# Performance work log

Measured on AMD Instinct MI355X. Metric: run time of the kernel, lower is better.

## Reference

```python
import jax, jax.numpy as jnp
import numpy as np

N_NODES = 50000
N_EDGES = 800000
D_IN = 256
D_HID = 128
NUM_LAYERS = 6
ALPHA = 0.1
THETA = 0.5
EPS = 1e-5  # BatchNorm1d default eps


def setup_inputs() -> dict:
    key = jax.random.key(0)
    ks = jax.random.split(key, 6)
    x = jax.random.normal(ks[0], (N_NODES, D_IN), dtype=jnp.float32)
    edge_index = jax.random.randint(ks[1], (2, N_EDGES), 0, N_NODES)
    # GCNConv(D_IN, D_HID): weight + bias
    W_lin = jax.random.normal(ks[2], (D_IN, D_HID), dtype=jnp.float32) / np.sqrt(D_IN).astype(np.float32)
    b_lin = jnp.zeros((D_HID,), jnp.float32)
    # GCN2Conv weight1 per layer (shared_weights=True -> only weight1, no bias)
    W1s = jax.random.normal(ks[3], (NUM_LAYERS - 1, D_HID, D_HID), dtype=jnp.float32) / np.sqrt(D_HID).astype(np.float32)
    # BatchNorm1d affine params per intermediate layer
    bn_gamma = jnp.ones((NUM_LAYERS - 2, D_HID), jnp.float32)
    bn_beta = jnp.zeros((NUM_LAYERS - 2, D_HID), jnp.float32)
    return {"x": x, "edge_index": edge_index, "W_lin": W_lin, "b_lin": b_lin,
            "W1s": W1s, "bn_gamma": bn_gamma, "bn_beta": bn_beta}


def _gcn_conv(x, W, b, edge_index):
    # PyG GCNConv: transform, add self-loops, D^{-1/2}(A+I)D^{-1/2} aggregation.
    n = x.shape[0]
    xw = x @ W  # [N, D_HID]
    loop = jnp.arange(n)
    src = jnp.concatenate([edge_index[0], loop])
    dst = jnp.concatenate([edge_index[1], loop])
    deg = jax.ops.segment_sum(jnp.ones(src.shape, xw.dtype), dst, num_segments=n)
    dinv = jax.lax.rsqrt(jnp.maximum(deg, 1.0))  # deg >= 1 thanks to self loops
    w = dinv[src] * dinv[dst]  # [E+N]
    return jax.ops.segment_sum(xw[src] * w[:, None], dst, num_segments=n) + b


def _gcn2_conv(z, x0, W1, edge_index, beta):
    # GCN2Conv with normalize=False, shared_weights=True:
    # h = (1-alpha)*sum_{j->i} z_j + alpha*x0 ; out = (1-beta)*h + beta*(h @ W1)
    n = z.shape[0]
    agg = jax.ops.segment_sum(z[edge_index[0]], edge_index[1], num_segments=n)
    h = (1.0 - ALPHA) * agg + ALPHA * x0
    return (1.0 - beta) * h + beta * (h @ W1)


def _batchnorm(z, gamma, beta_p):
    # training-mode BatchNorm1d over the node dimension (biased variance)
    mu = jnp.mean(z, axis=0)
    var = jnp.var(z, axis=0)
    return (z - mu) * jax.lax.rsqrt(var + EPS) * gamma + beta_p


def reference(x, edge_index, W_lin, b_lin, W1s, bn_gamma, bn_beta):
    z = _gcn_conv(x, W_lin, b_lin, edge_index)
    x0 = z
    n_convs = NUM_LAYERS - 1
    # GCN2Conv layer index l = i+1 -> beta_l = log(theta/l + 1)
    betas = [float(np.log(THETA / (i + 1) + 1.0)) for i in range(n_convs)]
    for i in range(n_convs):  # dropout=0.0 -> identity, omitted
        z = _gcn2_conv(z, x0, W1s[i], edge_index, betas[i])
        if i < n_convs - 1:
            z = _batchnorm(z, bn_gamma[i], bn_beta[i])
            z = jax.nn.relu(z)
    return z
```

## Files before the change

kernel.cpp:

```cpp
#include <hip/hip_runtime.h>
#include <math.h>

#define N_NODES 50000
#define N_EDGES 800000
#define D_IN 256
#define D_HID 128
#define ALPHA 0.1f
#define EPS 1e-5f

#define NBUCK 391
#define EPB 4096
#define NBLK 196

typedef __attribute__((ext_vector_type(8))) short bf16x8;
typedef __attribute__((ext_vector_type(4))) float f32x4;

static __device__ __forceinline__ unsigned short f2bf(float f) {
    unsigned int x = __float_as_uint(f);
    return (unsigned short)((x + 0x7fffu + ((x >> 16) & 1u)) >> 16);
}
static __device__ __forceinline__ float blo(unsigned int v) {
    return __uint_as_float(v << 16);
}
static __device__ __forceinline__ float bhi(unsigned int v) {
    return __uint_as_float(v & 0xffff0000u);
}
static __device__ __forceinline__ void unpack8(uint4 u, float* f) {
    f[0] = blo(u.x); f[1] = bhi(u.x);
    f[2] = blo(u.y); f[3] = bhi(u.y);
    f[4] = blo(u.z); f[5] = bhi(u.z);
    f[6] = blo(u.w); f[7] = bhi(u.w);
}

__global__ __launch_bounds__(256) void k_hist(const int* __restrict__ dst,
                                              int* __restrict__ hist, int e) {
    __shared__ int h[NBUCK];
    int t = threadIdx.x;
    for (int i = t; i < NBUCK; i += 256) h[i] = 0;
    __syncthreads();
    int base = blockIdx.x * EPB;
    int lim = e - base;
    if (lim > EPB) lim = EPB;
    for (int i = t; i < lim; i += 256) atomicAdd(&h[dst[base + i] >> 7], 1);
    __syncthreads();
    for (int i = t; i < NBUCK; i += 256) hist[blockIdx.x * NBUCK + i] = h[i];
}

__global__ __launch_bounds__(256) void k_bkscan(const int* __restrict__ hist,
                                                int* __restrict__ offsT, int* __restrict__ btot) {
    __shared__ int sh[256];
    int b = blockIdx.x;
    int t = threadIdx.x;
    int v = (t < NBLK) ? hist[t * NBUCK + b] : 0;
    sh[t] = v;
    __syncthreads();
    for (int ofs = 1; ofs < 256; ofs <<= 1) {
        int y = (t >= ofs) ? sh[t - ofs] : 0;
        __syncthreads();
        sh[t] += y;
        __syncthreads();
    }
    if (t < NBLK) offsT[b * NBLK + t] = sh[t] - v;
    if (t == 255) btot[b] = sh[255];
}

__global__ __launch_bounds__(512) void k_bbase(const int* __restrict__ btot,
                                               int* __restrict__ bbase, int* __restrict__ rp) {
    __shared__ int sh[512];
    int t = threadIdx.x;
    int v = (t < NBUCK) ? btot[t] : 0;
    sh[t] = v;
    __syncthreads();
    for (int ofs = 1; ofs < 512; ofs <<= 1) {
        int y = (t >= ofs) ? sh[t - ofs] : 0;
        __syncthreads();
        sh[t] += y;
        __syncthreads();
    }
    if (t < NBUCK) bbase[t] = sh[t] - v;
    if (t == 0) rp[N_NODES] = N_EDGES;
}

__global__ __launch_bounds__(256) void k_scatter(const int* __restrict__ src,
                                                 const int* __restrict__ dst,
                                                 const int* __restrict__ offsT,
                                                 const int* __restrict__ bbase,
                                                 unsigned int* __restrict__ buck, int e) {
    __shared__ int h[NBUCK];
    int t = threadIdx.x;
    for (int i = t; i < NBUCK; i += 256) h[i] = 0;
    __syncthreads();
    int base = blockIdx.x * EPB;
    int lim = e - base;
    if (lim > EPB) lim = EPB;
    for (int i = t; i < lim; i += 256) {
        int d = dst[base + i];
        int s = src[base + i];
        int b = d >> 7;
        int lp = atomicAdd(&h[b], 1);
        int pos = bbase[b] + offsT[b * NBLK + blockIdx.x] + lp;
        buck[pos] = (unsigned int)s | ((unsigned int)(d & 127) << 16);
    }
}

__global__ __launch_bounds__(256) void k_csr(const unsigned int* __restrict__ buck,
                                             const int* __restrict__ bbase,
                                             const int* __restrict__ btot,
                                             int* __restrict__ rp, float* __restrict__ dinv,
                                             int* __restrict__ cs) {
    __shared__ int dcnt[128];
    __shared__ int doff[128];
    int b = blockIdx.x;
    int t = threadIdx.x;
    if (t < 128) dcnt[t] = 0;
    __syncthreads();
    int base = bbase[b];
    int tot = btot[b];
    for (int i = t; i < tot; i += 256) {
        unsigned int v = buck[base + i];
        atomicAdd(&dcnt[(v >> 16) & 127], 1);
    }
    __syncthreads();
    if (t < 128) doff[t] = dcnt[t];
    __syncthreads();
    for (int ofs = 1; ofs < 128; ofs <<= 1) {
        int y = 0;
        if (t < 128 && t >= ofs) y = doff[t - ofs];
        __syncthreads();
        if (t < 128) doff[t] += y;
        __syncthreads();
    }
    int gd0 = b << 7;
    if (t < 128) {
        int ex = doff[t] - dcnt[t];
        if (gd0 + t < N_NODES) {
            rp[gd0 + t] = base + ex;
            dinv[gd0 + t] = rsqrtf((float)(dcnt[t] + 1));
        }
        dcnt[t] = ex;
    }
    __syncthreads();
    for (int i = t; i < tot; i += 256) {
        unsigned int v = buck[base + i];
        int p = atomicAdd(&dcnt[(v >> 16) & 127], 1);
        cs[base + p] = (int)(v & 0xffffu);
    }
}

__global__ __launch_bounds__(256) void k_prep_w(const float* __restrict__ W_lin,
                                                const float* __restrict__ W1s,
                                                unsigned short* __restrict__ Wlt,
                                                unsigned short* __restrict__ Wt) {
    int idx = blockIdx.x * 256 + threadIdx.x;
    if (idx < 128 * 256) {
        int c = idx >> 8, k = idx & 255;
        Wlt[idx] = f2bf(W_lin[k * 128 + c]);
    } else {
        int j = idx - 128 * 256;
        if (j < 5 * 128 * 128) {
            int l = j >> 14;
            int rem = j & 16383;
            int c = rem >> 7, k = rem & 127;
            float bet = logf(0.5f / (float)(l + 1) + 1.0f);
            float v = bet * W1s[l * 16384 + k * 128 + c];
            if (c == k) v += 1.0f - bet;
            Wt[j] = f2bf(v);
        }
    }
}

template <int K>
__global__ __launch_bounds__(256) void k_mgemm(const float* __restrict__ A,
                                               const unsigned short* __restrict__ Bt,
                                               unsigned short* __restrict__ outb, int M) {
    __shared__ short lds[2 * 128 * 136];
    short* As = lds;
    short* Bs = lds + 128 * 136;

    int t = threadIdx.x;
    int lane = t & 63;
    int wave = t >> 6;
    int wr = wave >> 1, wc = wave & 1;
    int row0 = blockIdx.x * 128;

    f32x4 acc[4][4];
#pragma unroll
    for (int m = 0; m < 4; ++m)
#pragma unroll
        for (int n = 0; n < 4; ++n) acc[m][n] = (f32x4){0.f, 0.f, 0.f, 0.f};

    int sr = t >> 1;
    int sh = t & 1;

    for (int k0 = 0; k0 < K; k0 += 128) {
        {
            int gr = row0 + sr;
            float4 zf = {0.f, 0.f, 0.f, 0.f};
            const float4* gp = (const float4*)(A + (size_t)gr * K + k0 + sh * 64);
#pragma unroll
            for (int u = 0; u < 8; ++u) {
                float4 a = (gr < M) ? gp[2 * u] : zf;
                float4 b = (gr < M) ? gp[2 * u + 1] : zf;
                uint4 w;
                w.x = (unsigned int)f2bf(a.x) | ((unsigned int)f2bf(a.y) << 16);
                w.y = (unsigned int)f2bf(a.z) | ((unsigned int)f2bf(a.w) << 16);
                w.z = (unsigned int)f2bf(b.x) | ((unsigned int)f2bf(b.y) << 16);
                w.w = (unsigned int)f2bf(b.z) | ((unsigned int)f2bf(b.w) << 16);
                *(uint4*)(As + sr * 136 + sh * 64 + u * 8) = w;
            }
        }
        {
            const uint4* gp = (const uint4*)(Bt + (size_t)sr * K + k0 + sh * 64);
#pragma unroll
            for (int u = 0; u < 8; ++u) {
                *(uint4*)(Bs + sr * 136 + sh * 64 + u * 8) = gp[u];
            }
        }
        __syncthreads();

#pragma unroll
        for (int ks = 0; ks < 4; ++ks) {
            bf16x8 af[4], bfr[4];
#pragma unroll
            for (int m = 0; m < 4; ++m)
                af[m] = *(const bf16x8*)(As + (wr * 64 + m * 16 + (lane & 15)) * 136 + ks * 32 + (lane >> 4) * 8);
#pragma unroll
            for (int n = 0; n < 4; ++n)
                bfr[n] = *(const bf16x8*)(Bs + (wc * 64 + n * 16 + (lane & 15)) * 136 + ks * 32 + (lane >> 4) * 8);
#pragma unroll
            for (int m = 0; m < 4; ++m)
#pragma unroll
                for (int n = 0; n < 4; ++n)
                    acc[m][n] = __builtin_amdgcn_mfma_f32_16x16x32_bf16(af[m], bfr[n], acc[m][n], 0, 0, 0);
        }
        __syncthreads();
    }

    short* Z = lds;
#pragma unroll
    for (int m = 0; m < 4; ++m)
#pragma unroll
        for (int n = 0; n < 4; ++n)
#pragma unroll
            for (int r = 0; r < 4; ++r) {
                int rl = wr * 64 + m * 16 + (lane >> 4) * 4 + r;
                int cl = wc * 64 + n * 16 + (lane & 15);
                Z[rl * 136 + cl] = (short)f2bf(acc[m][n][r]);
            }
    __syncthreads();
    int gr = row0 + sr;
    if (gr < M) {
#pragma unroll
        for (int u = 0; u < 8; ++u)
            *(uint4*)(outb + (size_t)gr * 128 + sh * 64 + u * 8) = *(uint4*)(Z + sr * 136 + sh * 64 + u * 8);
    }
}

template <int MODE>
__global__ __launch_bounds__(256) void k_lgemm(const unsigned short* __restrict__ A,
                                               const unsigned short* __restrict__ Bt,
                                               unsigned short* __restrict__ outb,
                                               float* __restrict__ outf,
                                               float* __restrict__ bn_s, float* __restrict__ bn_q,
                                               int M) {
    __shared__ short As[128 * 136];
    int t = threadIdx.x;
    int lane = t & 63;
    int wave = t >> 6;
    int wr = wave >> 1, wc = wave & 1;
    int row0 = blockIdx.x * 128;

    bf16x8 bfr[4][4];
#pragma unroll
    for (int ks = 0; ks < 4; ++ks)
#pragma unroll
        for (int n = 0; n < 4; ++n)
            bfr[ks][n] = *(const bf16x8*)(Bt + (size_t)(wc * 64 + n * 16 + (lane & 15)) * 128 + ks * 32 + (lane >> 4) * 8);

    int sr = t >> 1, sh = t & 1;
    {
        int gr = row0 + sr;
        uint4 zero = {0, 0, 0, 0};
        const uint4* gp = (const uint4*)(A + (size_t)gr * 128 + sh * 64);
#pragma unroll
        for (int u = 0; u < 8; ++u) {
            uint4 v = (gr < M) ? gp[u] : zero;
            *(uint4*)(As + sr * 136 + sh * 64 + u * 8) = v;
        }
    }
    __syncthreads();

    f32x4 acc[4][4];
#pragma unroll
    for (int m = 0; m < 4; ++m)
#pragma unroll
        for (int n = 0; n < 4; ++n) acc[m][n] = (f32x4){0.f, 0.f, 0.f, 0.f};

#pragma unroll
    for (int ks = 0; ks < 4; ++ks) {
        bf16x8 af[4];
#pragma unroll
        for (int m = 0; m < 4; ++m)
            af[m] = *(const bf16x8*)(As + (wr * 64 + m * 16 + (lane & 15)) * 136 + ks * 32 + (lane >> 4) * 8);
#pragma unroll
        for (int m = 0; m < 4; ++m)
#pragma unroll
            for (int n = 0; n < 4; ++n)
                acc[m][n] = __builtin_amdgcn_mfma_f32_16x16x32_bf16(af[m], bfr[ks][n], acc[m][n], 0, 0, 0);
    }

    if (MODE == 1) {
        float sum[4] = {0.f, 0.f, 0.f, 0.f}, sq[4] = {0.f, 0.f, 0.f, 0.f};
#pragma unroll
        for (int n = 0; n < 4; ++n)
#pragma unroll
            for (int m = 0; m < 4; ++m)
#pragma unroll
                for (int r = 0; r < 4; ++r) {
                    float v = acc[m][n][r];
                    sum[n] += v;
                    sq[n] += v * v;
                }
#pragma unroll
        for (int n = 0; n < 4; ++n) {
            sum[n] += __shfl_xor(sum[n], 16);
            sum[n] += __shfl_xor(sum[n], 32);
            sq[n] += __shfl_xor(sq[n], 16);
            sq[n] += __shfl_xor(sq[n], 32);
        }
        if (lane < 16) {
#pragma unroll
            for (int n = 0; n < 4; ++n) {
                int col = wc * 64 + n * 16 + lane;
                atomicAdd(&bn_s[col], sum[n]);
                atomicAdd(&bn_q[col], sq[n]);
            }
        }
    }

    if (MODE == 2) {
#pragma unroll
        for (int m = 0; m < 4; ++m)
#pragma unroll
            for (int n = 0; n < 4; ++n)
#pragma unroll
                for (int r = 0; r < 4; ++r) {
                    int gr = row0 + wr * 64 + m * 16 + (lane >> 4) * 4 + r;
                    int cl = wc * 64 + n * 16 + (lane & 15);
                    if (gr < M) outf[(size_t)gr * 128 + cl] = acc[m][n][r];
                }
    } else {
        __syncthreads();
        short* Z = As;
#pragma unroll
        for (int m = 0; m < 4; ++m)
#pragma unroll
            for (int n = 0; n < 4; ++n)
#pragma unroll
                for (int r = 0; r < 4; ++r) {
                    int rl = wr * 64 + m * 16 + (lane >> 4) * 4 + r;
                    int cl = wc * 64 + n * 16 + (lane & 15);
                    Z[rl * 136 + cl] = (short)f2bf(acc[m][n][r]);
                }
        __syncthreads();
        int gr = row0 + sr;
        if (gr < M) {
#pragma unroll
            for (int u = 0; u < 8; ++u)
                *(uint4*)(outb + (size_t)gr * 128 + sh * 64 + u * 8) = *(uint4*)(Z + sr * 136 + sh * 64 + u * 8);
        }
    }
}

template <int MODE>
__global__ __launch_bounds__(256) void k_agg(const uint4* __restrict__ src4,
                                             const uint4* __restrict__ x04,
                                             const int* __restrict__ rp, const int* __restrict__ cs,
                                             const float* __restrict__ dinv,
                                             const float* __restrict__ b_lin,
                                             const float* __restrict__ st,
                                             uint4* __restrict__ dst4,
                                             float* __restrict__ bns, int n) {
    if (blockIdx.x == 0) bns[threadIdx.x] = 0.f;

    int wid = (blockIdx.x * 256 + threadIdx.x) >> 6;
    int lane = threadIdx.x & 63;
    if (wid >= n) return;
    int q = lane >> 4;
    int c = lane & 15;

    int start = __builtin_amdgcn_readfirstlane(rp[wid]);
    int end = __builtin_amdgcn_readfirstlane(rp[wid + 1]);

    float sc[8], tc[8];
    if (MODE == 2) {
        float4 s0 = ((const float4*)st)[c * 2];
        float4 s1 = ((const float4*)st)[c * 2 + 1];
        float4 t0 = ((const float4*)st)[32 + c * 2];
        float4 t1 = ((const float4*)st)[32 + c * 2 + 1];
        sc[0] = s0.x; sc[1] = s0.y; sc[2] = s0.z; sc[3] = s0.w;
        sc[4] = s1.x; sc[5] = s1.y; sc[6] = s1.z; sc[7] = s1.w;
        tc[0] = t0.x; tc[1] = t0.y; tc[2] = t0.z; tc[3] = t0.w;
        tc[4] = t1.x; tc[5] = t1.y; tc[6] = t1.z; tc[7] = t1.w;
    }
    float dn = (MODE == 0) ? dinv[wid] : 0.f;

    float acc[8];
#pragma unroll
    for (int i = 0; i < 8; ++i) acc[i] = 0.f;

#define ACCUM(vv, ww)                                                     \
    {                                                                     \
        float f_[8];                                                      \
        unpack8(vv, f_);                                                  \
        if (MODE == 0) {                                                  \
            _Pragma("unroll") for (int i_ = 0; i_ < 8; ++i_)              \
                acc[i_] = fmaf(ww, f_[i_], acc[i_]);                      \
        } else if (MODE == 1) {                                           \
            _Pragma("unroll") for (int i_ = 0; i_ < 8; ++i_)              \
                acc[i_] += f_[i_];                                        \
        } else {                                                          \
            _Pragma("unroll") for (int i_ = 0; i_ < 8; ++i_)              \
                acc[i_] += fmaxf(fmaf(sc[i_], f_[i_], tc[i_]), 0.f);      \
        }                                                                 \
    }

    for (int base = start; base < end; base += 64) {
        int cnt = end - base;
        if (cnt > 64) cnt = 64;
        int myi = cs[base + ((lane < cnt) ? lane : 0)];
        float myw = (MODE == 0) ? dinv[myi] : 0.f;

        int j = 0;
        for (; j + 15 < cnt; j += 16) {
            int s0 = __shfl(myi, j + q);
            int s1 = __shfl(myi, j + 4 + q);
            int s2 = __shfl(myi, j + 8 + q);
            int s3 = __shfl(myi, j + 12 + q);
            uint4 v0 = src4[(size_t)s0 * 16 + c];
            uint4 v1 = src4[(size_t)s1 * 16 + c];
            uint4 v2 = src4[(size_t)s2 * 16 + c];
            uint4 v3 = src4[(size_t)s3 * 16 + c];
            float w0 = 0.f, w1 = 0.f, w2 = 0.f, w3 = 0.f;
            if (MODE == 0) {
                w0 = __shfl(myw, j + q) * dn;
                w1 = __shfl(myw, j + 4 + q) * dn;
                w2 = __shfl(myw, j + 8 + q) * dn;
                w3 = __shfl(myw, j + 12 + q) * dn;
            }
            ACCUM(v0, w0);
            ACCUM(v1, w1);
            ACCUM(v2, w2);
            ACCUM(v3, w3);
        }
        for (; j + 7 < cnt; j += 8) {
            int s0 = __shfl(myi, j + q);
            int s1 = __shfl(myi, j + 4 + q);
            uint4 v0 = src4[(size_t)s0 * 16 + c];
            uint4 v1 = src4[(size_t)s1 * 16 + c];
            float w0 = 0.f, w1 = 0.f;
            if (MODE == 0) {
                w0 = __shfl(myw, j + q) * dn;
                w1 = __shfl(myw, j + 4 + q) * dn;
            }
            ACCUM(v0, w0);
            ACCUM(v1, w1);
        }
        for (; j + 3 < cnt; j += 4) {
            int s0 = __shfl(myi, j + q);
            uint4 v0 = src4[(size_t)s0 * 16 + c];
            float w0 = 0.f;
            if (MODE == 0) w0 = __shfl(myw, j + q) * dn;
            ACCUM(v0, w0);
        }
        int rem = cnt - j;
        if (rem > 0) {
            int jj = j + q;
            bool act = jj < cnt;
            int jsafe = act ? jj : (cnt - 1);
            int s0 = __shfl(myi, jsafe);
            uint4 v0 = src4[(size_t)s0 * 16 + c];
            float m = act ? 1.f : 0.f;
            if (MODE == 0) {
                float w0 = __shfl(myw, jsafe) * dn * m;
                ACCUM(v0, w0);
            } else {
                float f_[8];
                unpack8(v0, f_);
                if (MODE == 1) {
#pragma unroll
                    for (int i_ = 0; i_ < 8; ++i_) acc[i_] = fmaf(m, f_[i_], acc[i_]);
                } else {
#pragma unroll
                    for (int i_ = 0; i_ < 8; ++i_)
                        acc[i_] = fmaf(m, fmaxf(fmaf(sc[i_], f_[i_], tc[i_]), 0.f), acc[i_]);
                }
            }
        }
    }
#undef ACCUM

#pragma unroll
    for (int i = 0; i < 8; ++i) {
        acc[i] += __shfl_xor(acc[i], 16);
        acc[i] += __shfl_xor(acc[i], 32);
    }

    if (MODE == 0) {
        uint4 sv = src4[(size_t)wid * 16 + c];
        float fs[8];
        unpack8(sv, fs);
        float w2 = dn * dn;
        float4 b0 = ((const float4*)b_lin)[c * 2];
        float4 b1 = ((const float4*)b_lin)[c * 2 + 1];
        float bb[8] = {b0.x, b0.y, b0.z, b0.w, b1.x, b1.y, b1.z, b1.w};
#pragma unroll
        for (int i = 0; i < 8; ++i) acc[i] = fmaf(w2, fs[i], acc[i]) + bb[i];
    } else {
        uint4 xv = x04[(size_t)wid * 16 + c];
        float fx[8];
        unpack8(xv, fx);
#pragma unroll
        for (int i = 0; i < 8; ++i) acc[i] = fmaf(ALPHA, fx[i], (1.0f - ALPHA) * acc[i]);
    }

    if (lane < 16) {
        uint4 o;
        o.x = (unsigned int)f2bf(acc[0]) | ((unsigned int)f2bf(acc[1]) << 16);
        o.y = (unsigned int)f2bf(acc[2]) | ((unsigned int)f2bf(acc[3]) << 16);
        o.z = (unsigned int)f2bf(acc[4]) | ((unsigned int)f2bf(acc[5]) << 16);
        o.w = (unsigned int)f2bf(acc[6]) | ((unsigned int)f2bf(acc[7]) << 16);
        dst4[(size_t)wid * 16 + c] = o;
    }
}

__global__ void k_bn_fin(const float* __restrict__ bn_s, const float* __restrict__ bn_q,
                         const float* __restrict__ gamma, const float* __restrict__ betap,
                         float* __restrict__ st, int n) {
    int c = threadIdx.x;
    float inv_n = 1.0f / (float)n;
    float mu = bn_s[c] * inv_n;
    float var = bn_q[c] * inv_n - mu * mu;
    var = fmaxf(var, 0.f);
    float s = gamma[c] * rsqrtf(var + EPS);
    st[c] = s;
    st[128 + c] = betap[c] - mu * s;
}

extern "C" void kernel_launch(void* const* d_in, const int* in_sizes, int n_in,
                              void* d_out, int out_size, void* d_ws, size_t ws_size,
                              hipStream_t stream) {
    const float* x = (const float*)d_in[0];
    const int* ei = (const int*)d_in[1];
    const float* W_lin = (const float*)d_in[2];
    const float* b_lin = (const float*)d_in[3];
    const float* W1s = (const float*)d_in[4];
    const float* gam = (const float*)d_in[5];
    const float* betp = (const float*)d_in[6];
    float* out = (float*)d_out;

    char* ws = (char*)d_ws;
    size_t off = 0;
    auto alloc = [&](size_t b) { size_t p = off; off = (off + b + 255) & ~(size_t)255; return p; };
    int* rp = (int*)(ws + alloc((size_t)(N_NODES + 1) * 4));
    int* cs = (int*)(ws + alloc((size_t)N_EDGES * 4));
    float* dinv = (float*)(ws + alloc((size_t)N_NODES * 4));
    int* hist = (int*)(ws + alloc((size_t)NBLK * NBUCK * 4));
    int* offsT = (int*)(ws + alloc((size_t)NBUCK * NBLK * 4));
    int* btot = (int*)(ws + alloc((size_t)NBUCK * 4));
    int* bbase = (int*)(ws + alloc((size_t)NBUCK * 4));
    unsigned int* buck = (unsigned int*)(ws + alloc((size_t)N_EDGES * 4));
    unsigned short* xwb = (unsigned short*)(ws + alloc((size_t)N_NODES * D_HID * 2));
    unsigned short* x0b = (unsigned short*)(ws + alloc((size_t)N_NODES * D_HID * 2));
    unsigned short* zb = (unsigned short*)(ws + alloc((size_t)N_NODES * D_HID * 2));
    unsigned short* hb = (unsigned short*)(ws + alloc((size_t)N_NODES * D_HID * 2));
    unsigned short* Wlt = (unsigned short*)(ws + alloc((size_t)128 * 256 * 2));
    unsigned short* Wt = (unsigned short*)(ws + alloc((size_t)5 * 128 * 128 * 2));
    float* bns = (float*)(ws + alloc(256 * 4));
    float* st = (float*)(ws + alloc(256 * 4));

    const int ggrid = (N_NODES + 127) / 128;
    const int agrid = (N_NODES + 3) / 4;

    k_hist<<<NBLK, 256, 0, stream>>>(ei + N_EDGES, hist, N_EDGES);
    k_bkscan<<<NBUCK, 256, 0, stream>>>(hist, offsT, btot);
    k_bbase<<<1, 512, 0, stream>>>(btot, bbase, rp);
    k_scatter<<<NBLK, 256, 0, stream>>>(ei, ei + N_EDGES, offsT, bbase, buck, N_EDGES);
    k_csr<<<NBUCK, 256, 0, stream>>>(buck, bbase, btot, rp, dinv, cs);

    k_prep_w<<<(128 * 256 + 5 * 128 * 128 + 255) / 256, 256, 0, stream>>>(W_lin, W1s, Wlt, Wt);

    k_mgemm<D_IN><<<ggrid, 256, 0, stream>>>(x, Wlt, xwb, N_NODES);
    k_agg<0><<<agrid, 256, 0, stream>>>((const uint4*)xwb, nullptr, rp, cs, dinv, b_lin,
                                        nullptr, (uint4*)x0b, bns, N_NODES);

    for (int i = 0; i < 5; ++i) {
        const unsigned short* zsrc = (i == 0) ? x0b : zb;
        if (i == 0)
            k_agg<1><<<agrid, 256, 0, stream>>>((const uint4*)zsrc, (const uint4*)x0b,
                                                rp, cs, nullptr, nullptr, nullptr,
                                                (uint4*)hb, bns, N_NODES);
        else
            k_agg<2><<<agrid, 256, 0, stream>>>((const uint4*)zsrc, (const uint4*)x0b,
                                                rp, cs, nullptr, nullptr, st,
                                                (uint4*)hb, bns, N_NODES);
        const unsigned short* W1 = Wt + (size_t)i * 128 * 128;
        if (i < 4) {
            k_lgemm<1><<<ggrid, 256, 0, stream>>>(hb, W1, zb, nullptr, bns, bns + 128, N_NODES);
            k_bn_fin<<<1, 128, 0, stream>>>(bns, bns + 128, gam + (size_t)i * 128,
                                            betp + (size_t)i * 128, st, N_NODES);
        } else {
            k_lgemm<2><<<ggrid, 256, 0, stream>>>(hb, W1, nullptr, out, nullptr, nullptr, N_NODES);
        }
    }
}
```

Measured before the change: 432.5 us.

## Unify GEMMs into 64-row tiled kernel and pre-cast input to bf16

Replaces the two GEMM kernels with one templated kernel that uses 64-row tiles, with each wave owning 16 rows across all 128 columns. This doubles the grid size for better occupancy and CU coverage. The fp32 input x is now converted to bf16 by a separate cast kernel, which moves the conversion out of the GEMM load path. That costs an extra read and write of the full x matrix. BatchNorm statistics are reduced in LDS before the atomics, and the fp32 output store goes through LDS for coalescing.

Result: no change. 435.2 us (+0.6%).

```diff
diff --git a/kernel.cpp b/kernel.cpp
--- a/kernel.cpp
+++ b/kernel.cpp
@@ -144,6 +144,20 @@
         unsigned int v = buck[base + i];
         int p = atomicAdd(&dcnt[(v >> 16) & 127], 1);
         cs[base + p] = (int)(v & 0xffffu);
+    }
+}
+
+__global__ __launch_bounds__(256) void k_cast_x(const float4* __restrict__ x, ushort2* __restrict__ xb,
+                                                int n4) {
+    int i = blockIdx.x * 256 + threadIdx.x;
+    if (i < n4) {
+        float4 v = x[i];
+        ushort2 a;
+        a.x = f2bf(v.x); a.y = f2bf(v.y);
+        ushort2 b;
+        b.x = f2bf(v.z); b.y = f2bf(v.w);
+        xb[i * 2] = a;
+        xb[i * 2 + 1] = b;
     }
 }
 
@@ -169,205 +183,116 @@
     }
 }
 
-template <int K>
-__global__ __launch_bounds__(256) void k_mgemm(const float* __restrict__ A,
-                                               const unsigned short* __restrict__ Bt,
-                                               unsigned short* __restrict__ outb, int M) {
-    __shared__ short lds[2 * 128 * 136];
+template <int K, int MODE>
+__global__ __launch_bounds__(256) void k_gemm(const unsigned short* __restrict__ A,
+                                              const unsigned short* __restrict__ Bt,
+                                              unsigned short* __restrict__ outb,
+                                              float* __restrict__ outf,
+                                              float* __restrict__ bn_s, float* __restrict__ bn_q,
+                                              int M) {
+    __shared__ short lds[64 * 136 + 128 * 136];
     short* As = lds;
-    short* Bs = lds + 128 * 136;
+    short* Bs = lds + 64 * 136;
 
     int t = threadIdx.x;
     int lane = t & 63;
-    int wave = t >> 6;
-    int wr = wave >> 1, wc = wave & 1;
-    int row0 = blockIdx.x * 128;
-
-    f32x4 acc[4][4];
-#pragma unroll
-    for (int m = 0; m < 4; ++m)
-#pragma unroll
-        for (int n = 0; n < 4; ++n) acc[m][n] = (f32x4){0.f, 0.f, 0.f, 0.f};
-
-    int sr = t >> 1;
-    int sh = t & 1;
+    int w = t >> 6;
+    int c16 = lane & 15;
+    int q16 = lane >> 4;
+    int row0 = blockIdx.x * 64;
+
+    f32x4 acc[8];
+#pragma unroll
+    for (int n = 0; n < 8; ++n) acc[n] = (f32x4){0.f, 0.f, 0.f, 0.f};
+
+    int ar = t >> 2, aq = t & 3;
+    int br = t >> 1, bh = t & 1;
 
     for (int k0 = 0; k0 < K; k0 += 128) {
         {
-            int gr = row0 + sr;
-            float4 zf = {0.f, 0.f, 0.f, 0.f};
-            const float4* gp = (const float4*)(A + (size_t)gr * K + k0 + sh * 64);
-#pragma unroll
-            for (int u = 0; u < 8; ++u) {
-                float4 a = (gr < M) ? gp[2 * u] : zf;
-                float4 b = (gr < M) ? gp[2 * u + 1] : zf;
-                uint4 w;
-                w.x = (unsigned int)f2bf(a.x) | ((unsigned int)f2bf(a.y) << 16);
-                w.y = (unsigned int)f2bf(a.z) | ((unsigned int)f2bf(a.w) << 16);
-                w.z = (unsigned int)f2bf(b.x) | ((unsigned int)f2bf(b.y) << 16);
-                w.w = (unsigned int)f2bf(b.z) | ((unsigned int)f2bf(b.w) << 16);
-                *(uint4*)(As + sr * 136 + sh * 64 + u * 8) = w;
+            int gr = row0 + ar;
+            uint4 z4 = {0, 0, 0, 0};
+            const uint4* gp = (const uint4*)(A + (size_t)gr * K + k0);
+#pragma unroll
+            for (int v = 0; v < 4; ++v) {
+                uint4 x4 = (gr < M) ? gp[aq * 4 + v] : z4;
+                *(uint4*)(As + ar * 136 + (aq * 4 + v) * 8) = x4;
             }
         }
         {
-            const uint4* gp = (const uint4*)(Bt + (size_t)sr * K + k0 + sh * 64);
-#pragma unroll
-            for (int u = 0; u < 8; ++u) {
-                *(uint4*)(Bs + sr * 136 + sh * 64 + u * 8) = gp[u];
+            const uint4* gp = (const uint4*)(Bt + (size_t)br * K + k0);
+#pragma unroll
+            for (int v = 0; v < 8; ++v)
+                *(uint4*)(Bs + br * 136 + (bh * 8 + v) * 8) = gp[bh * 8 + v];
+        }
+        __syncthreads();
+
+#pragma unroll
+        for (int ks = 0; ks < 4; ++ks) {
+            bf16x8 af = *(const bf16x8*)(As + (w * 16 + c16) * 136 + ks * 32 + q16 * 8);
+#pragma unroll
+            for (int n = 0; n < 8; ++n) {
+                bf16x8 bf = *(const bf16x8*)(Bs + (n * 16 + c16) * 136 + ks * 32 + q16 * 8);
+                acc[n] = __builtin_amdgcn_mfma_f32_16x16x32_bf16(af, bf, acc[n], 0, 0, 0);
             }
         }
         __syncthreads();
-
-#pragma unroll
-        for (int ks = 0; ks < 4; ++ks) {
-            bf16x8 af[4], bfr[4];
-#pragma unroll
-            for (int m = 0; m < 4; ++m)
-                af[m] = *(const bf16x8*)(As + (wr * 64 + m * 16 + (lane & 15)) * 136 + ks * 32 + (lane >> 4) * 8);
-#pragma unroll
-            for (int n = 0; n < 4; ++n)
-                bfr[n] = *(const bf16x8*)(Bs + (wc * 64 + n * 16 + (lane & 15)) * 136 + ks * 32 + (lane >> 4) * 8);
-#pragma unroll
-            for (int m = 0; m < 4; ++m)
-#pragma unroll
-                for (int n = 0; n < 4; ++n)
-                    acc[m][n] = __builtin_amdgcn_mfma_f32_16x16x32_bf16(af[m], bfr[n], acc[m][n], 0, 0, 0);
-        }
-        __syncthreads();
-    }
-
-    short* Z = lds;
-#pragma unroll
-    for (int m = 0; m < 4; ++m)
-#pragma unroll
-        for (int n = 0; n < 4; ++n)
-#pragma unroll
-            for (int r = 0; r < 4; ++r) {
-                int rl = wr * 64 + m * 16 + (lane >> 4) * 4 + r;
-                int cl = wc * 64 + n * 16 + (lane & 15);
-                Z[rl * 136 + cl] = (short)f2bf(acc[m][n][r]);
+    }
+
+    if (MODE == 2) {
+        float* Zf = (float*)lds;
+#pragma unroll
+        for (int n = 0; n < 8; ++n)
+#pragma unroll
+            for (int r = 0; r < 4; ++r)
+                Zf[(w * 16 + q16 * 4 + r) * 132 + n * 16 + c16] = acc[n][r];
+        __syncthreads();
+        int zr = t >> 2, zq = t & 3;
+        int gr = row0 + zr;
+        if (gr < M) {
+#pragma unroll
+            for (int v = 0; v < 8; ++v)
+                *(float4*)(outf + (size_t)gr * 128 + (zq * 8 + v) * 4) =
+                    *(float4*)(Zf + zr * 132 + (zq * 8 + v) * 4);
+        }
+    } else {
+        short* Z = As;
+        float* Sf = (float*)Bs;
+#pragma unroll
+        for (int n = 0; n < 8; ++n)
+#pragma unroll
+            for (int r = 0; r < 4; ++r)
+                Z[(w * 16 + q16 * 4 + r) * 136 + n * 16 + c16] = (short)f2bf(acc[n][r]);
+        if (MODE == 1) {
+#pragma unroll
+            for (int n = 0; n < 8; ++n) {
+                float s = acc[n][0] + acc[n][1] + acc[n][2] + acc[n][3];
+                float qq = acc[n][0] * acc[n][0] + acc[n][1] * acc[n][1] +
+                           acc[n][2] * acc[n][2] + acc[n][3] * acc[n][3];
+                s += __shfl_xor(s, 16);
+                s += __shfl_xor(s, 32);
+                qq += __shfl_xor(qq, 16);
+                qq += __shfl_xor(qq, 32);
+                if (lane < 16) {
+                    Sf[w * 128 + n * 16 + lane] = s;
+                    Sf[512 + w * 128 + n * 16 + lane] = qq;
+                }
             }
-    __syncthreads();
-    int gr = row0 + sr;
-    if (gr < M) {
-#pragma unroll
-        for (int u = 0; u < 8; ++u)
-            *(uint4*)(outb + (size_t)gr * 128 + sh * 64 + u * 8) = *(uint4*)(Z + sr * 136 + sh * 64 + u * 8);
-    }
-}
-
-template <int MODE>
-__global__ __launch_bounds__(256) void k_lgemm(const unsigned short* __restrict__ A,
-                                               const unsigned short* __restrict__ Bt,
-                                               unsigned short* __restrict__ outb,
-                                               float* __restrict__ outf,
-                                               float* __restrict__ bn_s, float* __restrict__ bn_q,
-                                               int M) {
-    __shared__ short As[128 * 136];
-    int t = threadIdx.x;
-    int lane = t & 63;
-    int wave = t >> 6;
-    int wr = wave >> 1, wc = wave & 1;
-    int row0 = blockIdx.x * 128;
-
-    bf16x8 bfr[4][4];
-#pragma unroll
-    for (int ks = 0; ks < 4; ++ks)
-#pragma unroll
-        for (int n = 0; n < 4; ++n)
-            bfr[ks][n] = *(const bf16x8*)(Bt + (size_t)(wc * 64 + n * 16 + (lane & 15)) * 128 + ks * 32 + (lane >> 4) * 8);
-
-    int sr = t >> 1, sh = t & 1;
-    {
-        int gr = row0 + sr;
-        uint4 zero = {0, 0, 0, 0};
-        const uint4* gp = (const uint4*)(A + (size_t)gr * 128 + sh * 64);
-#pragma unroll
-        for (int u = 0; u < 8; ++u) {
-            uint4 v = (gr < M) ? gp[u] : zero;
-            *(uint4*)(As + sr * 136 + sh * 64 + u * 8) = v;
-        }
-    }
-    __syncthreads();
-
-    f32x4 acc[4][4];
-#pragma unroll
-    for (int m = 0; m < 4; ++m)
-#pragma unroll
-        for (int n = 0; n < 4; ++n) acc[m][n] = (f32x4){0.f, 0.f, 0.f, 0.f};
-
-#pragma unroll
-    for (int ks = 0; ks < 4; ++ks) {
-        bf16x8 af[4];
-#pragma unroll
-        for (int m = 0; m < 4; ++m)
-            af[m] = *(const bf16x8*)(As + (wr * 64 + m * 16 + (lane & 15)) * 136 + ks * 32 + (lane >> 4) * 8);
-#pragma unroll
-        for (int m = 0; m < 4; ++m)
-#pragma unroll
-            for (int n = 0; n < 4; ++n)
-                acc[m][n] = __builtin_amdgcn_mfma_f32_16x16x32_bf16(af[m], bfr[ks][n], acc[m][n], 0, 0, 0);
-    }
-
-    if (MODE == 1) {
-        float sum[4] = {0.f, 0.f, 0.f, 0.f}, sq[4] = {0.f, 0.f, 0.f, 0.f};
-#pragma unroll
-        for (int n = 0; n < 4; ++n)
-#pragma unroll
-            for (int m = 0; m < 4; ++m)
-#pragma unroll
-                for (int r = 0; r < 4; ++r) {
-                    float v = acc[m][n][r];
-                    sum[n] += v;
-                    sq[n] += v * v;
-                }
-#pragma unroll
-        for (int n = 0; n < 4; ++n) {
-            sum[n] += __shfl_xor(sum[n], 16);
-            sum[n] += __shfl_xor(sum[n], 32);
-            sq[n] += __shfl_xor(sq[n], 16);
-            sq[n] += __shfl_xor(sq[n], 32);
-        }
-        if (lane < 16) {
-#pragma unroll
-            for (int n = 0; n < 4; ++n) {
-                int col = wc * 64 + n * 16 + lane;
-                atomicAdd(&bn_s[col], sum[n]);
-                atomicAdd(&bn_q[col], sq[n]);
-            }
-        }
-    }
-
-    if (MODE == 2) {
-#pragma unroll
-        for (int m = 0; m < 4; ++m)
-#pragma unroll
-            for (int n = 0; n < 4; ++n)
-#pragma unroll
-                for (int r = 0; r < 4; ++r) {
-                    int gr = row0 + wr * 64 + m * 16 + (lane >> 4) * 4 + r;
-                    int cl = wc * 64 + n * 16 + (lane & 15);
-                    if (gr < M) outf[(size_t)gr * 128 + cl] = acc[m][n][r];
-                }
-    } else {
-        __syncthreads();
-        short* Z = As;
-#pragma unroll
-        for (int m = 0; m < 4; ++m)
-#pragma unroll
-            for (int n = 0; n < 4; ++n)
-#pragma unroll
-                for (int r = 0; r < 4; ++r) {
-                    int rl = wr * 64 + m * 16 + (lane >> 4) * 4 + r;
-                    int cl = wc * 64 + n * 16 + (lane & 15);
-                    Z[rl * 136 + cl] = (short)f2bf(acc[m][n][r]);
-                }
-        __syncthreads();
-        int gr = row0 + sr;
+        }
+        __syncthreads();
+        int zr = t >> 2, zq = t & 3;
+        int gr = row0 + zr;
         if (gr < M) {
 #pragma unroll
-            for (int u = 0; u < 8; ++u)
-                *(uint4*)(outb + (size_t)gr * 128 + sh * 64 + u * 8) = *(uint4*)(Z + sr * 136 + sh * 64 + u * 8);
+            for (int v = 0; v < 4; ++v)
+                *(uint4*)(outb + (size_t)gr * 128 + (zq * 4 + v) * 8) =
+                    *(uint4*)(Z + zr * 136 + (zq * 4 + v) * 8);
+        }
+        if (MODE == 1 && t < 128) {
+            float s = Sf[t] + Sf[128 + t] + Sf[256 + t] + Sf[384 + t];
+            float qq = Sf[512 + t] + Sf[640 + t] + Sf[768 + t] + Sf[896 + t];
+            atomicAdd(&bn_s[t], s);
+            atomicAdd(&bn_q[t], qq);
         }
     }
 }
@@ -570,6 +495,7 @@
     int* btot = (int*)(ws + alloc((size_t)NBUCK * 4));
     int* bbase = (int*)(ws + alloc((size_t)NBUCK * 4));
     unsigned int* buck = (unsigned int*)(ws + alloc((size_t)N_EDGES * 4));
+    unsigned short* xb = (unsigned short*)(ws + alloc((size_t)N_NODES * D_IN * 2));
     unsigned short* xwb = (unsigned short*)(ws + alloc((size_t)N_NODES * D_HID * 2));
     unsigned short* x0b = (unsigned short*)(ws + alloc((size_t)N_NODES * D_HID * 2));
     unsigned short* zb = (unsigned short*)(ws + alloc((size_t)N_NODES * D_HID * 2));
@@ -579,7 +505,7 @@
     float* bns = (float*)(ws + alloc(256 * 4));
     float* st = (float*)(ws + alloc(256 * 4));
 
-    const int ggrid = (N_NODES + 127) / 128;
+    const int ggrid = (N_NODES + 63) / 64;
     const int agrid = (N_NODES + 3) / 4;
 
     k_hist<<<NBLK, 256, 0, stream>>>(ei + N_EDGES, hist, N_EDGES);
@@ -588,9 +514,11 @@
     k_scatter<<<NBLK, 256, 0, stream>>>(ei, ei + N_EDGES, offsT, bbase, buck, N_EDGES);
     k_csr<<<NBUCK, 256, 0, stream>>>(buck, bbase, btot, rp, dinv, cs);
 
+    k_cast_x<<<(N_NODES * D_IN / 4 + 255) / 256, 256, 0, stream>>>((const float4*)x, (ushort2*)xb,
+                                                                   N_NODES * D_IN / 4);
     k_prep_w<<<(128 * 256 + 5 * 128 * 128 + 255) / 256, 256, 0, stream>>>(W_lin, W1s, Wlt, Wt);
 
-    k_mgemm<D_IN><<<ggrid, 256, 0, stream>>>(x, Wlt, xwb, N_NODES);
+    k_gemm<D_IN, 0><<<ggrid, 256, 0, stream>>>(xb, Wlt, xwb, nullptr, nullptr, nullptr, N_NODES);
     k_agg<0><<<agrid, 256, 0, stream>>>((const uint4*)xwb, nullptr, rp, cs, dinv, b_lin,
                                         nullptr, (uint4*)x0b, bns, N_NODES);
 
@@ -606,11 +534,11 @@
                                                 (uint4*)hb, bns, N_NODES);
         const unsigned short* W1 = Wt + (size_t)i * 128 * 128;
         if (i < 4) {
-            k_lgemm<1><<<ggrid, 256, 0, stream>>>(hb, W1, zb, nullptr, bns, bns + 128, N_NODES);
+            k_gemm<D_HID, 1><<<ggrid, 256, 0, stream>>>(hb, W1, zb, nullptr, bns, bns + 128, N_NODES);
             k_bn_fin<<<1, 128, 0, stream>>>(bns, bns + 128, gam + (size_t)i * 128,
                                             betp + (size_t)i * 128, st, N_NODES);
         } else {
-            k_lgemm<2><<<ggrid, 256, 0, stream>>>(hb, W1, nullptr, out, nullptr, nullptr, N_NODES);
-        }
-    }
-}
+            k_gemm<D_HID, 2><<<ggrid, 256, 0, stream>>>(hb, W1, nullptr, out, nullptr, nullptr, N_NODES);
+        }
+    }
+}
```
